# Kernel optimization log

Hardware: AMD Instinct MI355X
Metric: run time of the kernel (lower is better)

Reference implementation:

```python
import jax, jax.numpy as jnp
import numpy as np

N = 100000
E = 1600000
IN_C = 256
HID = 256
OUT_C = 32
K = 2          # APPNP K = max(1, num_layers)
ALPHA = 0.1


def setup_inputs() -> dict:
    key = jax.random.key(0)
    ks = jax.random.split(key, 8)
    x = jax.random.normal(ks[0], (N, IN_C), dtype=jnp.float32)
    edge_index = jax.random.randint(ks[1], (2, E), 0, N, dtype=jnp.int64)
    s_in = 1.0 / np.sqrt(IN_C)
    s_h = 1.0 / np.sqrt(HID)
    W_in = jax.random.uniform(ks[2], (IN_C, HID), jnp.float32, -s_in, s_in)
    b_in = jax.random.uniform(ks[3], (HID,), jnp.float32, -s_in, s_in)
    W_h = jax.random.uniform(ks[4], (HID, HID), jnp.float32, -s_h, s_h)
    b_h = jax.random.uniform(ks[5], (HID,), jnp.float32, -s_h, s_h)
    W_out = jax.random.uniform(ks[6], (HID, OUT_C), jnp.float32, -s_h, s_h)
    b_out = jax.random.uniform(ks[7], (OUT_C,), jnp.float32, -s_h, s_h)
    return {"x": x, "edge_index": edge_index, "W_in": W_in, "b_in": b_in,
            "W_h": W_h, "b_h": b_h, "W_out": W_out, "b_out": b_out}


def _appnp(h0, src, dst):
    # gcn_norm with added self-loops: deg over destinations, sym normalization
    loops = jnp.arange(N, dtype=src.dtype)
    src_f = jnp.concatenate([src, loops])  # [E+N]
    dst_f = jnp.concatenate([dst, loops])
    deg = jax.ops.segment_sum(jnp.ones_like(dst_f, dtype=h0.dtype), dst_f,
                              num_segments=N)
    dinv = jnp.where(deg > 0, jax.lax.rsqrt(jnp.maximum(deg, 1e-12)), 0.0)
    norm = (dinv[src_f] * dinv[dst_f])[:, None]  # [E+N, 1]
    h = h0
    for _ in range(K):
        agg = jax.ops.segment_sum(h[src_f] * norm, dst_f, num_segments=N)
        h = (1.0 - ALPHA) * agg + ALPHA * h0
    return h


def reference(x, edge_index, W_in, b_in, W_h, b_h, W_out, b_out):
    # MLP encoder (dropout inactive in eval mode)
    h = jax.nn.relu(x @ W_in + b_in)
    h = jax.nn.relu(h @ W_h + b_h)
    h = h @ W_out + b_out  # [N, OUT_C]
    return _appnp(h, edge_index[0], edge_index[1])
```

## Files before the change

### kernel.cpp

```cpp
#include <hip/hip_runtime.h>

#define NN 100000
#define NE 1600000
#define NTILE 3125

#define BSH 7
#define BNODES 128
#define NBUCK 782
#define NBUCKP 784
#define CAP 2560
#define ECH 2048
#define NCHK 782

typedef _Float16 half8v __attribute__((ext_vector_type(8)));
typedef _Float16 half4v __attribute__((ext_vector_type(4)));
typedef float f32x4 __attribute__((ext_vector_type(4)));


__global__ __launch_bounds__(256) void k_count(const int* __restrict__ dst,
                                               int* __restrict__ histT) {
    __shared__ int h[NBUCKP];
    const int t = threadIdx.x;
    for (int b = t; b < NBUCKP; b += 256) h[b] = 0;
    __syncthreads();
    const int ebase = blockIdx.x * ECH + t * 8;
#pragma unroll
    for (int q = 0; q < 2; q++) {
        int e = ebase + q * 4;
        if (e + 4 <= NE) {
            int4 d4 = *reinterpret_cast<const int4*>(dst + e);
            atomicAdd(&h[d4.x >> BSH], 1);
            atomicAdd(&h[d4.y >> BSH], 1);
            atomicAdd(&h[d4.z >> BSH], 1);
            atomicAdd(&h[d4.w >> BSH], 1);
        } else {
            for (int p = e; p < NE; p++) atomicAdd(&h[dst[p] >> BSH], 1);
        }
    }
    __syncthreads();
    for (int b = t; b < NBUCK; b += 256) histT[(long long)b * NCHK + blockIdx.x] = h[b];
}

__global__ __launch_bounds__(256) void k_scanb(int* __restrict__ histT,
                                               int* __restrict__ cntb) {
    __shared__ int s[256];
    const int b = blockIdx.x, t = threadIdx.x;
    int* row = histT + (long long)b * NCHK;
    int v[4];
    int sum = 0;
#pragma unroll
    for (int j = 0; j < 4; j++) {
        int idx = t * 4 + j;
        v[j] = (idx < NCHK) ? row[idx] : 0;
        sum += v[j];
    }
    s[t] = sum;
    __syncthreads();
    for (int off = 1; off < 256; off <<= 1) {
        int u = (t >= off) ? s[t - off] : 0;
        __syncthreads();
        s[t] += u;
        __syncthreads();
    }
    int run = s[t] - sum;
#pragma unroll
    for (int j = 0; j < 4; j++) {
        int idx = t * 4 + j;
        if (idx < NCHK) row[idx] = run;
        run += v[j];
    }
    if (t == 255) cntb[b] = s[255];
}

__global__ __launch_bounds__(256) void k_part(const int* __restrict__ src,
                                              const int* __restrict__ dst,
                                              const int* __restrict__ histT,
                                              int* __restrict__ data) {
    __shared__ int curs[NBUCKP];
    const int t = threadIdx.x, blk = blockIdx.x;
    for (int b = t; b < NBUCKP; b += 256)
        curs[b] = b * CAP + ((b < NBUCK) ? histT[(long long)b * NCHK + blk] : 0);
    __syncthreads();
    const int ebase = blk * ECH + t * 8;
#pragma unroll
    for (int q = 0; q < 2; q++) {
        int e = ebase + q * 4;
        if (e + 4 <= NE) {
            int4 d4 = *reinterpret_cast<const int4*>(dst + e);
            int4 s4 = *reinterpret_cast<const int4*>(src + e);
            int p0 = atomicAdd(&curs[d4.x >> BSH], 1);
            data[p0] = (s4.x << BSH) | (d4.x & (BNODES - 1));
            int p1 = atomicAdd(&curs[d4.y >> BSH], 1);
            data[p1] = (s4.y << BSH) | (d4.y & (BNODES - 1));
            int p2 = atomicAdd(&curs[d4.z >> BSH], 1);
            data[p2] = (s4.z << BSH) | (d4.z & (BNODES - 1));
            int p3 = atomicAdd(&curs[d4.w >> BSH], 1);
            data[p3] = (s4.w << BSH) | (d4.w & (BNODES - 1));
        } else {
            for (int p = e; p < NE; p++) {
                int d = dst[p], sv = src[p];
                int pos = atomicAdd(&curs[d >> BSH], 1);
                data[pos] = (sv << BSH) | (d & (BNODES - 1));
            }
        }
    }
}

__global__ __launch_bounds__(256) void k_sortb(const int* __restrict__ data,
                                               const int* __restrict__ cntb,
                                               int* __restrict__ col,
                                               int* __restrict__ begp,
                                               int* __restrict__ endp,
                                               float* __restrict__ dinv) {
    __shared__ int hist[BNODES];
    __shared__ int scn[BNODES];
    __shared__ int curs[BNODES];
    const int b = blockIdx.x, t = threadIdx.x;
    if (t < BNODES) hist[t] = 0;
    __syncthreads();
    const int cnt = cntb[b];
    const int* wp = data + b * CAP;
    for (int e = t; e < cnt; e += 256) atomicAdd(&hist[wp[e] & (BNODES - 1)], 1);
    __syncthreads();
    if (t < BNODES) scn[t] = hist[t];
    __syncthreads();
    for (int off = 1; off < BNODES; off <<= 1) {
        int v = (t < BNODES && t >= off) ? scn[t - off] : 0;
        __syncthreads();
        if (t < BNODES) scn[t] += v;
        __syncthreads();
    }
    if (t < BNODES) {
        int beg = scn[t] - hist[t];
        curs[t] = beg;
        int node = (b << BSH) + t;
        if (node < NN) {
            begp[node] = b * CAP + beg;
            endp[node] = b * CAP + scn[t];
            dinv[node] = rsqrtf((float)(hist[t] + 1));
        }
    }
    __syncthreads();
    for (int e = t; e < cnt; e += 256) {
        int w = wp[e];
        int p = atomicAdd(&curs[w & (BNODES - 1)], 1);
        col[b * CAP + p] = w >> BSH;
    }
}


__device__ __forceinline__ void wfrag_one(const float* __restrict__ W,
                                          _Float16* __restrict__ Wf, int idx, int N) {
    int j = idx & 7;
    int l = (idx >> 3) & 63;
    int f = idx >> 9;
    int nt = f % (N / 16);
    int kt = f / (N / 16);
    int k = kt * 32 + (l >> 4) * 8 + j;
    int c = nt * 16 + (l & 15);
    Wf[idx] = (_Float16)W[k * N + c];
}

__global__ __launch_bounds__(256) void k_wfrag_all(const float* __restrict__ W1,
                                                   const float* __restrict__ W2,
                                                   const float* __restrict__ W3,
                                                   _Float16* __restrict__ Wf1,
                                                   _Float16* __restrict__ Wf2,
                                                   _Float16* __restrict__ Wf3) {
    int idx = blockIdx.x * 256 + threadIdx.x;
    if (idx < 65536) wfrag_one(W1, Wf1, idx, 256);
    else if (idx < 131072) wfrag_one(W2, Wf2, idx - 65536, 256);
    else if (idx < 139264) wfrag_one(W3, Wf3, idx - 131072, 32);
}


__global__ __launch_bounds__(512) void k_lay1(const float* __restrict__ x,
                                              const _Float16* __restrict__ Wf1,
                                              const float* __restrict__ b1,
                                              _Float16* __restrict__ h1g) {
    __shared__ char buf[32 * 512];
    const int t = threadIdx.x;
    const int lane = t & 63;
    const int G = lane >> 4;
    const int w = t >> 6;
    const int T = blockIdx.x;

    half8v wr[8][2];
    {
        const half8v* W1f = reinterpret_cast<const half8v*>(Wf1);
#pragma unroll
        for (int kt = 0; kt < 8; kt++)
#pragma unroll
            for (int n2 = 0; n2 < 2; n2++)
                wr[kt][n2] = W1f[(kt * 16 + 2 * w + n2) * 64 + lane];
    }
    float bvs[2];
#pragma unroll
    for (int n2 = 0; n2 < 2; n2++) bvs[n2] = b1[w * 32 + n2 * 16 + (lane & 15)];

    {
        const float4* A4 = reinterpret_cast<const float4*>(x + (size_t)T * 32 * 256);
#pragma unroll
        for (int i = t; i < 2048; i += 512) {
            int r = i >> 6, c4 = i & 63;
            float4 v = A4[i];
            half4v hv;
            hv[0] = (_Float16)v.x; hv[1] = (_Float16)v.y;
            hv[2] = (_Float16)v.z; hv[3] = (_Float16)v.w;
            int bo = (r * 512 + c4 * 8) ^ ((r & 7) << 4);
            *reinterpret_cast<half4v*>(buf + bo) = hv;
        }
    }
    __syncthreads();

    f32x4 acc[2][2];
#pragma unroll
    for (int mt = 0; mt < 2; mt++)
#pragma unroll
        for (int n2 = 0; n2 < 2; n2++) acc[mt][n2] = (f32x4)0.f;
#pragma unroll
    for (int kt = 0; kt < 8; kt++) {
        half8v a[2];
#pragma unroll
        for (int mt = 0; mt < 2; mt++) {
            int row = mt * 16 + (lane & 15);
            int bo = (row * 512 + kt * 64 + (G << 4)) ^ ((row & 7) << 4);
            a[mt] = *reinterpret_cast<const half8v*>(buf + bo);
        }
#pragma unroll
        for (int mt = 0; mt < 2; mt++)
#pragma unroll
            for (int n2 = 0; n2 < 2; n2++)
                acc[mt][n2] = __builtin_amdgcn_mfma_f32_16x16x32_f16(a[mt], wr[kt][n2], acc[mt][n2], 0, 0, 0);
    }
    __syncthreads();

#pragma unroll
    for (int mt = 0; mt < 2; mt++)
#pragma unroll
        for (int n2 = 0; n2 < 2; n2++) {
            int colc = w * 32 + n2 * 16 + (lane & 15);
            float bb = bvs[n2];
#pragma unroll
            for (int r = 0; r < 4; r++) {
                int row = mt * 16 + G * 4 + r;
                float v = fmaxf(acc[mt][n2][r] + bb, 0.f);
                int bo = (row * 512 + colc * 2) ^ ((row & 7) << 4);
                *reinterpret_cast<_Float16*>(buf + bo) = (_Float16)v;
            }
        }
    __syncthreads();

    {
        half8v* dst = reinterpret_cast<half8v*>(h1g + (size_t)T * 8192);
        const half8v* srcp = reinterpret_cast<const half8v*>(buf);
#pragma unroll
        for (int i = t; i < 1024; i += 512) dst[i] = srcp[i];
    }
}


__global__ __launch_bounds__(512) void k_lay23(const _Float16* __restrict__ h1g,
                                               const _Float16* __restrict__ Wf2,
                                               const _Float16* __restrict__ Wf3,
                                               const float* __restrict__ b2,
                                               const float* __restrict__ b3,
                                               const float* __restrict__ dinv,
                                               _Float16* __restrict__ h0f,
                                               _Float16* __restrict__ hs0) {
    __shared__ char buf[32 * 512];
    const int t = threadIdx.x;
    const int lane = t & 63;
    const int G = lane >> 4;
    const int w = t >> 6;
    const int T = blockIdx.x;

    half8v wr[8][2];
    {
        const half8v* W2f = reinterpret_cast<const half8v*>(Wf2);
#pragma unroll
        for (int kt = 0; kt < 8; kt++)
#pragma unroll
            for (int n2 = 0; n2 < 2; n2++)
                wr[kt][n2] = W2f[(kt * 16 + 2 * w + n2) * 64 + lane];
    }
    float bvs[2];
#pragma unroll
    for (int n2 = 0; n2 < 2; n2++) bvs[n2] = b2[w * 32 + n2 * 16 + (lane & 15)];

    {
        const half8v* srcp = reinterpret_cast<const half8v*>(h1g + (size_t)T * 8192);
        half8v* dst = reinterpret_cast<half8v*>(buf);
#pragma unroll
        for (int i = t; i < 1024; i += 512) dst[i] = srcp[i];
    }
    __syncthreads();

    f32x4 acc[2][2];
#pragma unroll
    for (int mt = 0; mt < 2; mt++)
#pragma unroll
        for (int n2 = 0; n2 < 2; n2++) acc[mt][n2] = (f32x4)0.f;
#pragma unroll
    for (int kt = 0; kt < 8; kt++) {
        half8v a[2];
#pragma unroll
        for (int mt = 0; mt < 2; mt++) {
            int row = mt * 16 + (lane & 15);
            int bo = (row * 512 + kt * 64 + (G << 4)) ^ ((row & 7) << 4);
            a[mt] = *reinterpret_cast<const half8v*>(buf + bo);
        }
#pragma unroll
        for (int mt = 0; mt < 2; mt++)
#pragma unroll
            for (int n2 = 0; n2 < 2; n2++)
                acc[mt][n2] = __builtin_amdgcn_mfma_f32_16x16x32_f16(a[mt], wr[kt][n2], acc[mt][n2], 0, 0, 0);
    }
    __syncthreads();

#pragma unroll
    for (int mt = 0; mt < 2; mt++)
#pragma unroll
        for (int n2 = 0; n2 < 2; n2++) {
            int colc = w * 32 + n2 * 16 + (lane & 15);
            float bb = bvs[n2];
#pragma unroll
            for (int r = 0; r < 4; r++) {
                int row = mt * 16 + G * 4 + r;
                float v = fmaxf(acc[mt][n2][r] + bb, 0.f);
                int bo = (row * 512 + colc * 2) ^ ((row & 7) << 4);
                *reinterpret_cast<_Float16*>(buf + bo) = (_Float16)v;
            }
        }
    __syncthreads();

    if (w < 4) {
        const half8v* W3f = reinterpret_cast<const half8v*>(Wf3);
        const int mt3 = w >> 1, ct3 = w & 1;
        const float bb3 = b3[ct3 * 16 + (lane & 15)];
        f32x4 a3 = (f32x4)0.f;
#pragma unroll
        for (int kt = 0; kt < 8; kt++) {
            int row = mt3 * 16 + (lane & 15);
            int bo = (row * 512 + kt * 64 + (G << 4)) ^ ((row & 7) << 4);
            half8v a = *reinterpret_cast<const half8v*>(buf + bo);
            half8v b = W3f[(kt * 2 + ct3) * 64 + lane];
            a3 = __builtin_amdgcn_mfma_f32_16x16x32_f16(a, b, a3, 0, 0, 0);
        }
        int colc = ct3 * 16 + (lane & 15);
#pragma unroll
        for (int r = 0; r < 4; r++) {
            size_t row = (size_t)T * 32 + mt3 * 16 + G * 4 + r;
            float v = a3[r] + bb3;
            h0f[row * 32 + colc] = (_Float16)v;
            hs0[row * 32 + colc] = (_Float16)(dinv[row] * v);
        }
    }
}


template<bool FINAL>
__global__ __launch_bounds__(256) void k_appnp(const int* __restrict__ begp,
                                               const int* __restrict__ endp,
                                               const int* __restrict__ col,
                                               const float* __restrict__ dinv,
                                               const _Float16* __restrict__ hs,
                                               const _Float16* __restrict__ h0f,
                                               void* __restrict__ outp) {
    int node = blockIdx.x * 4 + (threadIdx.x >> 6);
    if (node >= NN) return;
    const int lane = threadIdx.x & 63;
    const int slot = lane >> 2;
    const int cg = lane & 3;

    const int beg = begp[node];
    const int end = endp[node];
    const float dd = dinv[node];
    const half8v selfv = *reinterpret_cast<const half8v*>(hs + (size_t)node * 32 + cg * 8);
    const half8v h0v = *reinterpret_cast<const half8v*>(h0f + (size_t)node * 32 + cg * 8);

    float acc[8];
#pragma unroll
    for (int j = 0; j < 8; j++) acc[j] = 0.f;

    for (int e = beg + slot; e < end; e += 16) {
        int s = col[e];
        half8v v = *reinterpret_cast<const half8v*>(hs + (size_t)s * 32 + cg * 8);
#pragma unroll
        for (int j = 0; j < 8; j++) acc[j] += (float)v[j];
    }

#pragma unroll
    for (int off = 4; off < 64; off <<= 1) {
#pragma unroll
        for (int j = 0; j < 8; j++) acc[j] += __shfl_xor(acc[j], off, 64);
    }

    if (slot == 0) {
        float o[8];
#pragma unroll
        for (int j = 0; j < 8; j++)
            o[j] = 0.9f * dd * (acc[j] + (float)selfv[j]) + 0.1f * (float)h0v[j];
        size_t off = (size_t)node * 32 + cg * 8;
        if (FINAL) {
            float4 v0 = make_float4(o[0], o[1], o[2], o[3]);
            float4 v1 = make_float4(o[4], o[5], o[6], o[7]);
            float4* op = reinterpret_cast<float4*>((float*)outp + off);
            op[0] = v0; op[1] = v1;
        } else {
            half8v hv;
#pragma unroll
            for (int j = 0; j < 8; j++) hv[j] = (_Float16)(dd * o[j]);
            *reinterpret_cast<half8v*>((_Float16*)outp + off) = hv;
        }
    }
}


extern "C" void kernel_launch(void* const* d_in, const int* in_sizes, int n_in,
                              void* d_out, int out_size, void* d_ws, size_t ws_size,
                              hipStream_t stream) {
    const float* x     = (const float*)d_in[0];
    const int*   ei    = (const int*)d_in[1];
    const float* W_in  = (const float*)d_in[2];
    const float* b_in  = (const float*)d_in[3];
    const float* W_h   = (const float*)d_in[4];
    const float* b_h   = (const float*)d_in[5];
    const float* W_out = (const float*)d_in[6];
    const float* b_out = (const float*)d_in[7];
    float* out = (float*)d_out;

    const int* srcv = ei;
    const int* dstv = ei + NE;

    char* ws = (char*)d_ws;
    _Float16* h0f  = (_Float16*)ws;
    _Float16* hs0  = h0f + (size_t)NN * 32;
    _Float16* hs1  = hs0 + (size_t)NN * 32;
    float* dinv    = (float*)(hs1 + (size_t)NN * 32);
    _Float16* Wf_in  = (_Float16*)(dinv + NN);
    _Float16* Wf_h   = Wf_in + 256 * 256;
    _Float16* Wf_out = Wf_h + 256 * 256;
    _Float16* h1g    = Wf_out + 256 * 32;
    int* histT = (int*)(h1g + (size_t)NN * 256);
    int* cntb  = histT + (size_t)NBUCK * NCHK;
    int* data  = cntb + NBUCKP;
    int* col   = data + (size_t)NBUCKP * CAP;
    int* begp  = col + (size_t)NBUCKP * CAP;
    int* endp  = begp + NN;

    k_count<<<NCHK, 256, 0, stream>>>(dstv, histT);
    k_scanb<<<NBUCK, 256, 0, stream>>>(histT, cntb);
    k_part<<<NCHK, 256, 0, stream>>>(srcv, dstv, histT, data);
    k_sortb<<<NBUCK, 256, 0, stream>>>(data, cntb, col, begp, endp, dinv);

    k_wfrag_all<<<544, 256, 0, stream>>>(W_in, W_h, W_out, Wf_in, Wf_h, Wf_out);

    k_lay1<<<NTILE, 512, 0, stream>>>(x, Wf_in, b_in, h1g);
    k_lay23<<<NTILE, 512, 0, stream>>>(h1g, Wf_h, Wf_out, b_h, b_out, dinv, h0f, hs0);

    k_appnp<false><<<(NN + 3) / 4, 256, 0, stream>>>(begp, endp, col, dinv, hs0, h0f, hs1);
    k_appnp<true ><<<(NN + 3) / 4, 256, 0, stream>>>(begp, endp, col, dinv, hs1, h0f, out);
}
```

Baseline: 182.1 us.

## Fuse graph-partition kernels with weight prep and layer-1 GEMM via block specialization

Merges the destination-bucket count kernel with the weight fragment conversion, and the edge partition kernel with the first MLP layer, using blockIdx ranges to pick which role a block plays. Chunk size grows from 2048 to 8192 edges (196 chunks), so the per-bucket scan becomes one element per thread and the histogram matrix shrinks. This cuts two launches and lets the irregular edge work overlap with the dense GEMM. In exchange the larger edge chunks give fewer, longer-running partition blocks and more shared-memory atomic contention per block.

```diff
diff --git a/kernel.cpp b/kernel.cpp
--- a/kernel.cpp
+++ b/kernel.cpp
@@ -9,23 +9,51 @@
 #define NBUCK 782
 #define NBUCKP 784
 #define CAP 2560
-#define ECH 2048
-#define NCHK 782
+#define ECH 8192
+#define NCHK 196
+#define WFRAG_BLKS 272
 
 typedef _Float16 half8v __attribute__((ext_vector_type(8)));
 typedef _Float16 half4v __attribute__((ext_vector_type(4)));
 typedef float f32x4 __attribute__((ext_vector_type(4)));
 
 
-__global__ __launch_bounds__(256) void k_count(const int* __restrict__ dst,
-                                               int* __restrict__ histT) {
+__device__ __forceinline__ void wfrag_one(const float* __restrict__ W,
+                                          _Float16* __restrict__ Wf, int idx, int N) {
+    int j = idx & 7;
+    int l = (idx >> 3) & 63;
+    int f = idx >> 9;
+    int nt = f % (N / 16);
+    int kt = f / (N / 16);
+    int k = kt * 32 + (l >> 4) * 8 + j;
+    int c = nt * 16 + (l & 15);
+    Wf[idx] = (_Float16)W[k * N + c];
+}
+
+
+__global__ __launch_bounds__(512) void k_count_wfrag(const int* __restrict__ dst,
+                                                     int* __restrict__ histT,
+                                                     const float* __restrict__ W1,
+                                                     const float* __restrict__ W2,
+                                                     const float* __restrict__ W3,
+                                                     _Float16* __restrict__ Wf1,
+                                                     _Float16* __restrict__ Wf2,
+                                                     _Float16* __restrict__ Wf3) {
+    const int t = threadIdx.x;
+    if (blockIdx.x >= NCHK) {
+        int idx = (blockIdx.x - NCHK) * 512 + t;
+        if (idx < 65536) wfrag_one(W1, Wf1, idx, 256);
+        else if (idx < 131072) wfrag_one(W2, Wf2, idx - 65536, 256);
+        else if (idx < 139264) wfrag_one(W3, Wf3, idx - 131072, 32);
+        return;
+    }
     __shared__ int h[NBUCKP];
-    const int t = threadIdx.x;
-    for (int b = t; b < NBUCKP; b += 256) h[b] = 0;
-    __syncthreads();
-    const int ebase = blockIdx.x * ECH + t * 8;
-#pragma unroll
-    for (int q = 0; q < 2; q++) {
+    const int blk = blockIdx.x;
+    for (int b = t; b < NBUCKP; b += 512) h[b] = 0;
+    __syncthreads();
+    const int ebase = blk * ECH + t * 16;
+#pragma unroll
+    for (int q = 0; q < 4; q++) {
         int e = ebase + q * 4;
         if (e + 4 <= NE) {
             int4 d4 = *reinterpret_cast<const int4*>(dst + e);
@@ -35,26 +63,21 @@
             atomicAdd(&h[d4.w >> BSH], 1);
         } else {
             for (int p = e; p < NE; p++) atomicAdd(&h[dst[p] >> BSH], 1);
-        }
-    }
-    __syncthreads();
-    for (int b = t; b < NBUCK; b += 256) histT[(long long)b * NCHK + blockIdx.x] = h[b];
-}
+            break;
+        }
+    }
+    __syncthreads();
+    for (int b = t; b < NBUCK; b += 512) histT[(long long)b * NCHK + blk] = h[b];
+}
+
 
 __global__ __launch_bounds__(256) void k_scanb(int* __restrict__ histT,
                                                int* __restrict__ cntb) {
     __shared__ int s[256];
     const int b = blockIdx.x, t = threadIdx.x;
     int* row = histT + (long long)b * NCHK;
-    int v[4];
-    int sum = 0;
-#pragma unroll
-    for (int j = 0; j < 4; j++) {
-        int idx = t * 4 + j;
-        v[j] = (idx < NCHK) ? row[idx] : 0;
-        sum += v[j];
-    }
-    s[t] = sum;
+    int v = (t < NCHK) ? row[t] : 0;
+    s[t] = v;
     __syncthreads();
     for (int off = 1; off < 256; off <<= 1) {
         int u = (t >= off) ? s[t - off] : 0;
@@ -62,49 +85,135 @@
         s[t] += u;
         __syncthreads();
     }
-    int run = s[t] - sum;
-#pragma unroll
-    for (int j = 0; j < 4; j++) {
-        int idx = t * 4 + j;
-        if (idx < NCHK) row[idx] = run;
-        run += v[j];
-    }
+    if (t < NCHK) row[t] = s[t] - v;
     if (t == 255) cntb[b] = s[255];
 }
 
-__global__ __launch_bounds__(256) void k_part(const int* __restrict__ src,
-                                              const int* __restrict__ dst,
-                                              const int* __restrict__ histT,
-                                              int* __restrict__ data) {
-    __shared__ int curs[NBUCKP];
-    const int t = threadIdx.x, blk = blockIdx.x;
-    for (int b = t; b < NBUCKP; b += 256)
-        curs[b] = b * CAP + ((b < NBUCK) ? histT[(long long)b * NCHK + blk] : 0);
-    __syncthreads();
-    const int ebase = blk * ECH + t * 8;
-#pragma unroll
-    for (int q = 0; q < 2; q++) {
-        int e = ebase + q * 4;
-        if (e + 4 <= NE) {
-            int4 d4 = *reinterpret_cast<const int4*>(dst + e);
-            int4 s4 = *reinterpret_cast<const int4*>(src + e);
-            int p0 = atomicAdd(&curs[d4.x >> BSH], 1);
-            data[p0] = (s4.x << BSH) | (d4.x & (BNODES - 1));
-            int p1 = atomicAdd(&curs[d4.y >> BSH], 1);
-            data[p1] = (s4.y << BSH) | (d4.y & (BNODES - 1));
-            int p2 = atomicAdd(&curs[d4.z >> BSH], 1);
-            data[p2] = (s4.z << BSH) | (d4.z & (BNODES - 1));
-            int p3 = atomicAdd(&curs[d4.w >> BSH], 1);
-            data[p3] = (s4.w << BSH) | (d4.w & (BNODES - 1));
-        } else {
-            for (int p = e; p < NE; p++) {
-                int d = dst[p], sv = src[p];
-                int pos = atomicAdd(&curs[d >> BSH], 1);
-                data[pos] = (sv << BSH) | (d & (BNODES - 1));
+
+__global__ __launch_bounds__(512) void k_part_lay1(const int* __restrict__ src,
+                                                   const int* __restrict__ dst,
+                                                   const int* __restrict__ histT,
+                                                   int* __restrict__ data,
+                                                   const float* __restrict__ x,
+                                                   const _Float16* __restrict__ Wf1,
+                                                   const float* __restrict__ b1,
+                                                   _Float16* __restrict__ h1g) {
+    __shared__ char smem[16384];
+    const int t = threadIdx.x;
+
+    if (blockIdx.x < NCHK) {
+        int* curs = (int*)smem;
+        const int blk = blockIdx.x;
+        for (int b = t; b < NBUCKP; b += 512)
+            curs[b] = b * CAP + ((b < NBUCK) ? histT[(long long)b * NCHK + blk] : 0);
+        __syncthreads();
+        const int ebase = blk * ECH + t * 16;
+#pragma unroll
+        for (int q = 0; q < 4; q++) {
+            int e = ebase + q * 4;
+            if (e + 4 <= NE) {
+                int4 d4 = *reinterpret_cast<const int4*>(dst + e);
+                int4 s4 = *reinterpret_cast<const int4*>(src + e);
+                int p0 = atomicAdd(&curs[d4.x >> BSH], 1);
+                data[p0] = (s4.x << BSH) | (d4.x & (BNODES - 1));
+                int p1 = atomicAdd(&curs[d4.y >> BSH], 1);
+                data[p1] = (s4.y << BSH) | (d4.y & (BNODES - 1));
+                int p2 = atomicAdd(&curs[d4.z >> BSH], 1);
+                data[p2] = (s4.z << BSH) | (d4.z & (BNODES - 1));
+                int p3 = atomicAdd(&curs[d4.w >> BSH], 1);
+                data[p3] = (s4.w << BSH) | (d4.w & (BNODES - 1));
+            } else {
+                for (int p = e; p < NE; p++) {
+                    int d = dst[p], sv = src[p];
+                    int pos = atomicAdd(&curs[d >> BSH], 1);
+                    data[pos] = (sv << BSH) | (d & (BNODES - 1));
+                }
+                break;
             }
         }
-    }
-}
+        return;
+    }
+
+    char* buf = smem;
+    const int lane = t & 63;
+    const int G = lane >> 4;
+    const int w = t >> 6;
+    const int T = blockIdx.x - NCHK;
+
+    half8v wr[8][2];
+    {
+        const half8v* W1f = reinterpret_cast<const half8v*>(Wf1);
+#pragma unroll
+        for (int kt = 0; kt < 8; kt++)
+#pragma unroll
+            for (int n2 = 0; n2 < 2; n2++)
+                wr[kt][n2] = W1f[(kt * 16 + 2 * w + n2) * 64 + lane];
+    }
+    float bvs[2];
+#pragma unroll
+    for (int n2 = 0; n2 < 2; n2++) bvs[n2] = b1[w * 32 + n2 * 16 + (lane & 15)];
+
+    {
+        const float4* A4 = reinterpret_cast<const float4*>(x + (size_t)T * 32 * 256);
+#pragma unroll
+        for (int i = t; i < 2048; i += 512) {
+            int r = i >> 6, c4 = i & 63;
+            float4 v = A4[i];
+            half4v hv;
+            hv[0] = (_Float16)v.x; hv[1] = (_Float16)v.y;
+            hv[2] = (_Float16)v.z; hv[3] = (_Float16)v.w;
+            int bo = (r * 512 + c4 * 8) ^ ((r & 7) << 4);
+            *reinterpret_cast<half4v*>(buf + bo) = hv;
+        }
+    }
+    __syncthreads();
+
+    f32x4 acc[2][2];
+#pragma unroll
+    for (int mt = 0; mt < 2; mt++)
+#pragma unroll
+        for (int n2 = 0; n2 < 2; n2++) acc[mt][n2] = (f32x4)0.f;
+#pragma unroll
+    for (int kt = 0; kt < 8; kt++) {
+        half8v a[2];
+#pragma unroll
+        for (int mt = 0; mt < 2; mt++) {
+            int row = mt * 16 + (lane & 15);
+            int bo = (row * 512 + kt * 64 + (G << 4)) ^ ((row & 7) << 4);
+            a[mt] = *reinterpret_cast<const half8v*>(buf + bo);
+        }
+#pragma unroll
+        for (int mt = 0; mt < 2; mt++)
+#pragma unroll
+            for (int n2 = 0; n2 < 2; n2++)
+                acc[mt][n2] = __builtin_amdgcn_mfma_f32_16x16x32_f16(a[mt], wr[kt][n2], acc[mt][n2], 0, 0, 0);
+    }
+    __syncthreads();
+
+#pragma unroll
+    for (int mt = 0; mt < 2; mt++)
+#pragma unroll
+        for (int n2 = 0; n2 < 2; n2++) {
+            int colc = w * 32 + n2 * 16 + (lane & 15);
+            float bb = bvs[n2];
+#pragma unroll
+            for (int r = 0; r < 4; r++) {
+                int row = mt * 16 + G * 4 + r;
+                float v = fmaxf(acc[mt][n2][r] + bb, 0.f);
+                int bo = (row * 512 + colc * 2) ^ ((row & 7) << 4);
+                *reinterpret_cast<_Float16*>(buf + bo) = (_Float16)v;
+            }
+        }
+    __syncthreads();
+
+    {
+        half8v* dstp = reinterpret_cast<half8v*>(h1g + (size_t)T * 8192);
+        const half8v* srcp = reinterpret_cast<const half8v*>(buf);
+#pragma unroll
+        for (int i = t; i < 1024; i += 512) dstp[i] = srcp[i];
+    }
+}
+
 
 __global__ __launch_bounds__(256) void k_sortb(const int* __restrict__ data,
                                                const int* __restrict__ cntb,
@@ -145,117 +254,6 @@
         int w = wp[e];
         int p = atomicAdd(&curs[w & (BNODES - 1)], 1);
         col[b * CAP + p] = w >> BSH;
-    }
-}
-
-
-__device__ __forceinline__ void wfrag_one(const float* __restrict__ W,
-                                          _Float16* __restrict__ Wf, int idx, int N) {
-    int j = idx & 7;
-    int l = (idx >> 3) & 63;
-    int f = idx >> 9;
-    int nt = f % (N / 16);
-    int kt = f / (N / 16);
-    int k = kt * 32 + (l >> 4) * 8 + j;
-    int c = nt * 16 + (l & 15);
-    Wf[idx] = (_Float16)W[k * N + c];
-}
-
-__global__ __launch_bounds__(256) void k_wfrag_all(const float* __restrict__ W1,
-                                                   const float* __restrict__ W2,
-                                                   const float* __restrict__ W3,
-                                                   _Float16* __restrict__ Wf1,
-                                                   _Float16* __restrict__ Wf2,
-                                                   _Float16* __restrict__ Wf3) {
-    int idx = blockIdx.x * 256 + threadIdx.x;
-    if (idx < 65536) wfrag_one(W1, Wf1, idx, 256);
-    else if (idx < 131072) wfrag_one(W2, Wf2, idx - 65536, 256);
-    else if (idx < 139264) wfrag_one(W3, Wf3, idx - 131072, 32);
-}
-
-
-__global__ __launch_bounds__(512) void k_lay1(const float* __restrict__ x,
-                                              const _Float16* __restrict__ Wf1,
-                                              const float* __restrict__ b1,
-                                              _Float16* __restrict__ h1g) {
-    __shared__ char buf[32 * 512];
-    const int t = threadIdx.x;
-    const int lane = t & 63;
-    const int G = lane >> 4;
-    const int w = t >> 6;
-    const int T = blockIdx.x;
-
-    half8v wr[8][2];
-    {
-        const half8v* W1f = reinterpret_cast<const half8v*>(Wf1);
-#pragma unroll
-        for (int kt = 0; kt < 8; kt++)
-#pragma unroll
-            for (int n2 = 0; n2 < 2; n2++)
-                wr[kt][n2] = W1f[(kt * 16 + 2 * w + n2) * 64 + lane];
-    }
-    float bvs[2];
-#pragma unroll
-    for (int n2 = 0; n2 < 2; n2++) bvs[n2] = b1[w * 32 + n2 * 16 + (lane & 15)];
-
-    {
-        const float4* A4 = reinterpret_cast<const float4*>(x + (size_t)T * 32 * 256);
-#pragma unroll
-        for (int i = t; i < 2048; i += 512) {
-            int r = i >> 6, c4 = i & 63;
-            float4 v = A4[i];
-            half4v hv;
-            hv[0] = (_Float16)v.x; hv[1] = (_Float16)v.y;
-            hv[2] = (_Float16)v.z; hv[3] = (_Float16)v.w;
-            int bo = (r * 512 + c4 * 8) ^ ((r & 7) << 4);
-            *reinterpret_cast<half4v*>(buf + bo) = hv;
-        }
-    }
-    __syncthreads();
-
-    f32x4 acc[2][2];
-#pragma unroll
-    for (int mt = 0; mt < 2; mt++)
-#pragma unroll
-        for (int n2 = 0; n2 < 2; n2++) acc[mt][n2] = (f32x4)0.f;
-#pragma unroll
-    for (int kt = 0; kt < 8; kt++) {
-        half8v a[2];
-#pragma unroll
-        for (int mt = 0; mt < 2; mt++) {
-            int row = mt * 16 + (lane & 15);
-            int bo = (row * 512 + kt * 64 + (G << 4)) ^ ((row & 7) << 4);
-            a[mt] = *reinterpret_cast<const half8v*>(buf + bo);
-        }
-#pragma unroll
-        for (int mt = 0; mt < 2; mt++)
-#pragma unroll
-            for (int n2 = 0; n2 < 2; n2++)
-                acc[mt][n2] = __builtin_amdgcn_mfma_f32_16x16x32_f16(a[mt], wr[kt][n2], acc[mt][n2], 0, 0, 0);
-    }
-    __syncthreads();
-
-#pragma unroll
-    for (int mt = 0; mt < 2; mt++)
-#pragma unroll
-        for (int n2 = 0; n2 < 2; n2++) {
-            int colc = w * 32 + n2 * 16 + (lane & 15);
-            float bb = bvs[n2];
-#pragma unroll
-            for (int r = 0; r < 4; r++) {
-                int row = mt * 16 + G * 4 + r;
-                float v = fmaxf(acc[mt][n2][r] + bb, 0.f);
-                int bo = (row * 512 + colc * 2) ^ ((row & 7) << 4);
-                *reinterpret_cast<_Float16*>(buf + bo) = (_Float16)v;
-            }
-        }
-    __syncthreads();
-
-    {
-        half8v* dst = reinterpret_cast<half8v*>(h1g + (size_t)T * 8192);
-        const half8v* srcp = reinterpret_cast<const half8v*>(buf);
-#pragma unroll
-        for (int i = t; i < 1024; i += 512) dst[i] = srcp[i];
     }
 }
 
@@ -290,9 +288,9 @@
 
     {
         const half8v* srcp = reinterpret_cast<const half8v*>(h1g + (size_t)T * 8192);
-        half8v* dst = reinterpret_cast<half8v*>(buf);
-#pragma unroll
-        for (int i = t; i < 1024; i += 512) dst[i] = srcp[i];
+        half8v* dstp = reinterpret_cast<half8v*>(buf);
+#pragma unroll
+        for (int i = t; i < 1024; i += 512) dstp[i] = srcp[i];
     }
     __syncthreads();
 
@@ -449,14 +447,16 @@
     int* begp  = col + (size_t)NBUCKP * CAP;
     int* endp  = begp + NN;
 
-    k_count<<<NCHK, 256, 0, stream>>>(dstv, histT);
+    k_count_wfrag<<<NCHK + WFRAG_BLKS, 512, 0, stream>>>(dstv, histT,
+                                                         W_in, W_h, W_out,
+                                                         Wf_in, Wf_h, Wf_out);
     k_scanb<<<NBUCK, 256, 0, stream>>>(histT, cntb);
-    k_part<<<NCHK, 256, 0, stream>>>(srcv, dstv, histT, data);
+
+    k_part_lay1<<<NCHK + NTILE, 512, 0, stream>>>(srcv, dstv, histT, data,
+                                                  x, Wf_in, b_in, h1g);
+
     k_sortb<<<NBUCK, 256, 0, stream>>>(data, cntb, col, begp, endp, dinv);
 
-    k_wfrag_all<<<544, 256, 0, stream>>>(W_in, W_h, W_out, Wf_in, Wf_h, Wf_out);
-
-    k_lay1<<<NTILE, 512, 0, stream>>>(x, Wf_in, b_in, h1g);
     k_lay23<<<NTILE, 512, 0, stream>>>(h1g, Wf_h, Wf_out, b_h, b_out, dinv, h0f, hs0);
 
     k_appnp<false><<<(NN + 3) / 4, 256, 0, stream>>>(begp, endp, col, dinv, hs0, h0f, hs1);
```

Result: faster. 166.1 us (-8.8%).
